# Kernel optimization log

Hardware: AMD Instinct MI355X
Metric: run time of the kernel (lower is better)

Reference implementation:

```python
import jax, jax.numpy as jnp
import numpy as np

N = 100000      # nodes
E = 800000      # edges (avg degree 8)
D_IN = 128
D_OUT = 128
HOPS = 3        # K in SGConv


def setup_inputs() -> dict:
    key = jax.random.key(0)
    k1, k2, k3 = jax.random.split(key, 3)
    x = jax.random.normal(k1, (N, D_IN), dtype=jnp.float32)
    edge_index = jax.random.randint(k2, (2, E), 0, N, dtype=jnp.int64)
    # SGConv's final torch.nn.Linear(in_channels, out_channels)
    W = jax.random.normal(k3, (D_OUT, D_IN), dtype=jnp.float32) / np.sqrt(D_IN).astype(np.float32)
    b = jnp.zeros((D_OUT,), dtype=jnp.float32)
    return {"x": x, "edge_index": edge_index, "W": W, "b": b}


def reference(x, edge_index, W, b):
    n = x.shape[0]
    loop = jnp.arange(n, dtype=edge_index.dtype)
    # gcn_norm with add_self_loops=True (SGConv default)
    src = jnp.concatenate([edge_index[0], loop])  # message sources
    dst = jnp.concatenate([edge_index[1], loop])  # aggregation targets
    ones = jnp.ones(src.shape[0], dtype=x.dtype)
    deg = jax.ops.segment_sum(ones, dst, num_segments=n)
    dinv = jnp.where(deg > 0, jax.lax.rsqrt(deg), 0.0)
    norm = dinv[src] * dinv[dst]  # symmetric D^-1/2 A_hat D^-1/2 coefficients

    def hop(h, _):
        msg = h[src] * norm[:, None]                      # [E+N, D] gather
        return jax.ops.segment_sum(msg, dst, num_segments=n), None

    h, _ = jax.lax.scan(hop, x, None, length=HOPS)        # A_norm^K x
    return h @ W.T + b                                     # final linear
```

## Files before the change

kernel.cpp:

```cpp
#include <hip/hip_runtime.h>
#include <hip/hip_bf16.h>

#define DF 128


typedef __attribute__((ext_vector_type(8))) short shortx8;
typedef __attribute__((ext_vector_type(4))) float floatx4;

__device__ __forceinline__ unsigned short f32_to_bf16_rne(float f) {
    unsigned int u = __float_as_uint(f);
    unsigned int r = (u >> 16) & 1u;
    u += 0x7FFFu + r;
    return (unsigned short)(u >> 16);
}
__device__ __forceinline__ float bf16_lo(unsigned int w) { return __uint_as_float(w << 16); }
__device__ __forceinline__ float bf16_hi(unsigned int w) { return __uint_as_float(w & 0xffff0000u); }
__device__ __forceinline__ unsigned int pack_bf16(float x, float y) {
    return ((unsigned int)f32_to_bf16_rne(y) << 16) | (unsigned int)f32_to_bf16_rne(x);
}

__global__ void detect_flags_kernel(const unsigned int* __restrict__ ew, int enwords,
                                    const unsigned short* __restrict__ xh, int xnh,
                                    int* __restrict__ flagI, int* __restrict__ flagD) {
    __shared__ int eodd_nz;
    __shared__ int xbig;
    if (threadIdx.x == 0) { eodd_nz = 0; xbig = 0; }
    __syncthreads();
    int f1 = 0;
    for (int i = 1 + 2 * (int)threadIdx.x; i < enwords; i += 2 * (int)blockDim.x)
        if (ew[i] != 0u) f1 = 1;
    int c = 0;
    for (int i = 2 * (int)threadIdx.x; i < xnh; i += 2 * (int)blockDim.x) {
        unsigned int e = ((unsigned int)xh[i] >> 7) & 0xFFu;
        if (e >= 0xC0u) c++;
    }
    if (f1) eodd_nz = 1;
    if (c) atomicAdd(&xbig, c);
    __syncthreads();
    if (threadIdx.x == 0) {
        *flagI = (eodd_nz == 0) ? 1 : 0;
        *flagD = (xbig > 8) ? 0 : 1;
    }
}

__global__ __launch_bounds__(256) void prep_kernel(
        const int* __restrict__ eidx, const int* __restrict__ flagI,
        const int* __restrict__ flagD, int E, int n,
        int* __restrict__ cnt, int* __restrict__ rank,
        const void* __restrict__ x, uint2* __restrict__ xb, int nw2,
        const void* __restrict__ W, const void* __restrict__ b,
        unsigned short* __restrict__ Wb, float* __restrict__ bias_f,
        int g1, int g2) {
    int bid = (int)blockIdx.x;
    if (bid < g1) {
        int t = bid * 256 + (int)threadIdx.x;
        int base = t * 4;
        if (base >= E) return;
        int isI64 = *flagI;
        const long long* p64 = (const long long*)eidx;
        int s[4], d[4];
#pragma unroll
        for (int j = 0; j < 4; ++j) {
            int e = base + j;
            if (e < E) {
                if (isI64) { s[j] = (int)p64[e]; d[j] = (int)p64[(long long)E + e]; }
                else       { s[j] = eidx[e];     d[j] = eidx[E + e]; }
            } else { s[j] = -1; d[j] = -1; }
        }
        int r[4];
#pragma unroll
        for (int j = 0; j < 4; ++j) {
            bool ok = ((unsigned)d[j] < (unsigned)n) && ((unsigned)s[j] < (unsigned)n);
            r[j] = ok ? atomicAdd(&cnt[d[j]], 1) : 0;
        }
        if (base + 3 < E) {
            *(int4*)&rank[base] = make_int4(r[0], r[1], r[2], r[3]);
        } else {
#pragma unroll
            for (int j = 0; j < 4; ++j)
                if (base + j < E) rank[base + j] = r[j];
        }
    } else if (bid < g1 + g2) {
        int i = (bid - g1) * 256 + (int)threadIdx.x;
        if (i >= nw2) return;
        if (*flagD) {
            xb[i] = ((const uint2*)x)[i];
        } else {
            float4 v = ((const float4*)x)[i];
            uint2 o;
            o.x = pack_bf16(v.x, v.y);
            o.y = pack_bf16(v.z, v.w);
            xb[i] = o;
        }
    } else {
        int i = (bid - g1 - g2) * 256 + (int)threadIdx.x;
        int bf = *flagD;
        if (i < 128 * 128)
            Wb[i] = bf ? ((const unsigned short*)W)[i] : f32_to_bf16_rne(((const float*)W)[i]);
        if (i < 128)
            bias_f[i] = bf ? bf16_lo((unsigned int)((const unsigned short*)b)[i]) : ((const float*)b)[i];
    }
}

__global__ void scan_blocks_kernel(const int* __restrict__ cnt, int* __restrict__ row_start,
                                   int* __restrict__ partials, int n) {
    __shared__ int s[256];
    int i = blockIdx.x * 256 + threadIdx.x;
    int v = (i < n) ? cnt[i] : 0;
    s[threadIdx.x] = v;
    __syncthreads();
    for (int off = 1; off < 256; off <<= 1) {
        int t = ((int)threadIdx.x >= off) ? s[threadIdx.x - off] : 0;
        __syncthreads();
        s[threadIdx.x] += t;
        __syncthreads();
    }
    if (i < n) row_start[i] = s[threadIdx.x] - v;
    if (threadIdx.x == 255) partials[blockIdx.x] = s[255];
}

__global__ void scan_partials_kernel(int* __restrict__ partials, int nparts) {
    __shared__ int s[512];
    int v = ((int)threadIdx.x < nparts) ? partials[threadIdx.x] : 0;
    s[threadIdx.x] = v;
    __syncthreads();
    for (int off = 1; off < 512; off <<= 1) {
        int t = ((int)threadIdx.x >= off) ? s[threadIdx.x - off] : 0;
        __syncthreads();
        s[threadIdx.x] += t;
        __syncthreads();
    }
    if ((int)threadIdx.x < nparts) partials[threadIdx.x] = s[threadIdx.x] - v;
}

__global__ void finalize_rows_kernel(int* __restrict__ row_start, const int* __restrict__ partials,
                                     const int* __restrict__ cnt, float* __restrict__ dinv, int n) {
    int i = blockIdx.x * 256 + threadIdx.x;
    if (i < n) {
        int r = row_start[i] + partials[blockIdx.x];
        row_start[i] = r;
        dinv[i] = rsqrtf((float)(cnt[i] + 1));
        if (i == n - 1) row_start[n] = r + cnt[i];
    }
}

__global__ __launch_bounds__(256) void scatter_kernel(const int* __restrict__ eidx,
                                                      const int* __restrict__ flagI,
                                                      const int* __restrict__ rank,
                                                      const int* __restrict__ row_start,
                                                      int E, int n, const float* __restrict__ dinv,
                                                      int2* __restrict__ csr) {
    int t = blockIdx.x * blockDim.x + threadIdx.x;
    int base = t * 4;
    if (base >= E) return;
    int isI64 = *flagI;
    const long long* p64 = (const long long*)eidx;
    int s[4], d[4], r[4];
    if (base + 3 < E) {
        int4 rv = *(const int4*)&rank[base];
        r[0] = rv.x; r[1] = rv.y; r[2] = rv.z; r[3] = rv.w;
#pragma unroll
        for (int j = 0; j < 4; ++j) {
            int e = base + j;
            if (isI64) { s[j] = (int)p64[e]; d[j] = (int)p64[(long long)E + e]; }
            else       { s[j] = eidx[e];     d[j] = eidx[E + e]; }
        }
    } else {
#pragma unroll
        for (int j = 0; j < 4; ++j) {
            int e = base + j;
            if (e < E) {
                r[j] = rank[e];
                if (isI64) { s[j] = (int)p64[e]; d[j] = (int)p64[(long long)E + e]; }
                else       { s[j] = eidx[e];     d[j] = eidx[E + e]; }
            } else { s[j] = -1; d[j] = -1; r[j] = 0; }
        }
    }
#pragma unroll
    for (int j = 0; j < 4; ++j) {
        bool ok = ((unsigned)d[j] < (unsigned)n) && ((unsigned)s[j] < (unsigned)n);
        if (ok) {
            int pos = row_start[d[j]] + r[j];
            int2 pk;
            pk.x = s[j];
            pk.y = __float_as_int(dinv[s[j]]);
            csr[pos] = pk;
        }
    }
}

__global__ __launch_bounds__(256) void hop_kernel(const uint4* __restrict__ hin,
                                                  uint4* __restrict__ hout,
                                                  const int2* __restrict__ csr,
                                                  const int* __restrict__ row_start,
                                                  const float* __restrict__ dinv, int n) {
    int gw = (int)((blockIdx.x * 256 + threadIdx.x) >> 6);
    int lane = (int)(threadIdx.x & 63);
    if (gw >= n) return;
    int e = lane >> 4, c = lane & 15;
    float di = dinv[gw];
    int beg = row_start[gw], end = row_start[gw + 1];
    uint4 sv = hin[(size_t)gw * 16 + c];
    float a0 = 0.f, a1 = 0.f, a2 = 0.f, a3 = 0.f, a4 = 0.f, a5 = 0.f, a6 = 0.f, a7 = 0.f;
    for (int j = beg + e; j < end; j += 8) {
        int2 ed0 = csr[j];
        bool has1 = (j + 4) < end;
        int2 ed1 = has1 ? csr[j + 4] : ed0;
        uint4 v0 = hin[(size_t)ed0.x * 16 + c];
        uint4 v1 = hin[(size_t)ed1.x * 16 + c];
        float w0 = __int_as_float(ed0.y);
        float w1 = has1 ? __int_as_float(ed1.y) : 0.f;
        a0 += w0 * bf16_lo(v0.x); a1 += w0 * bf16_hi(v0.x);
        a2 += w0 * bf16_lo(v0.y); a3 += w0 * bf16_hi(v0.y);
        a4 += w0 * bf16_lo(v0.z); a5 += w0 * bf16_hi(v0.z);
        a6 += w0 * bf16_lo(v0.w); a7 += w0 * bf16_hi(v0.w);
        a0 += w1 * bf16_lo(v1.x); a1 += w1 * bf16_hi(v1.x);
        a2 += w1 * bf16_lo(v1.y); a3 += w1 * bf16_hi(v1.y);
        a4 += w1 * bf16_lo(v1.z); a5 += w1 * bf16_hi(v1.z);
        a6 += w1 * bf16_lo(v1.w); a7 += w1 * bf16_hi(v1.w);
    }
    a0 += __shfl_xor(a0, 16); a0 += __shfl_xor(a0, 32);
    a1 += __shfl_xor(a1, 16); a1 += __shfl_xor(a1, 32);
    a2 += __shfl_xor(a2, 16); a2 += __shfl_xor(a2, 32);
    a3 += __shfl_xor(a3, 16); a3 += __shfl_xor(a3, 32);
    a4 += __shfl_xor(a4, 16); a4 += __shfl_xor(a4, 32);
    a5 += __shfl_xor(a5, 16); a5 += __shfl_xor(a5, 32);
    a6 += __shfl_xor(a6, 16); a6 += __shfl_xor(a6, 32);
    a7 += __shfl_xor(a7, 16); a7 += __shfl_xor(a7, 32);
    a0 = di * (a0 + di * bf16_lo(sv.x)); a1 = di * (a1 + di * bf16_hi(sv.x));
    a2 = di * (a2 + di * bf16_lo(sv.y)); a3 = di * (a3 + di * bf16_hi(sv.y));
    a4 = di * (a4 + di * bf16_lo(sv.z)); a5 = di * (a5 + di * bf16_hi(sv.z));
    a6 = di * (a6 + di * bf16_lo(sv.w)); a7 = di * (a7 + di * bf16_hi(sv.w));
    if (e == 0) {
        uint4 o;
        o.x = pack_bf16(a0, a1);
        o.y = pack_bf16(a2, a3);
        o.z = pack_bf16(a4, a5);
        o.w = pack_bf16(a6, a7);
        hout[(size_t)gw * 16 + c] = o;
    }
}

__global__ __launch_bounds__(256, 2) void linear_mfma_kernel(
        const unsigned short* __restrict__ h, const unsigned short* __restrict__ Wb,
        const float* __restrict__ bias_f, void* __restrict__ out,
        const int* __restrict__ flagD, int n) {
    int bf = *flagD;
    int wave = (int)(threadIdx.x >> 6);
    int lane = (int)(threadIdx.x & 63);
    int q = lane >> 4, m16 = lane & 15;

    shortx8 bfrag[8][4];
    float bias[8];
#pragma unroll
    for (int nt = 0; nt < 8; ++nt) {
        int wr = nt * 16 + m16;
#pragma unroll
        for (int t = 0; t < 4; ++t)
            bfrag[nt][t] = *(const shortx8*)&Wb[wr * 128 + t * 32 + q * 8];
        bias[nt] = bias_f[wr];
    }

    int nstrips = (n + 15) / 16;
    int wid = (int)blockIdx.x * 4 + wave;
    int nw = (int)gridDim.x * 4;
    for (int s = wid; s < nstrips; s += nw) {
        int row0 = s * 16;
        int arow = row0 + m16;
        if (arow >= n) arow = n - 1;
        shortx8 afrag[4];
#pragma unroll
        for (int t = 0; t < 4; ++t)
            afrag[t] = *(const shortx8*)&h[(size_t)arow * 128 + t * 32 + q * 8];

        floatx4 acc[8];
#pragma unroll
        for (int nt = 0; nt < 8; ++nt) acc[nt] = (floatx4){0.f, 0.f, 0.f, 0.f};
#pragma unroll
        for (int t = 0; t < 4; ++t)
#pragma unroll
            for (int nt = 0; nt < 8; ++nt)
                acc[nt] = __builtin_amdgcn_mfma_f32_16x16x32_bf16(afrag[t], bfrag[nt][t], acc[nt], 0, 0, 0);

#pragma unroll
        for (int nt = 0; nt < 8; ++nt)
#pragma unroll
            for (int r = 0; r < 4; ++r) {
                int row = row0 + q * 4 + r;
                if (row < n) {
                    float v = acc[nt][r] + bias[nt];
                    size_t oi = (size_t)row * 128 + nt * 16 + m16;
                    if (bf) ((unsigned short*)out)[oi] = f32_to_bf16_rne(v);
                    else    ((float*)out)[oi] = v;
                }
            }
    }
}

extern "C" void kernel_launch(void* const* d_in, const int* in_sizes, int n_in,
                              void* d_out, int out_size, void* d_ws, size_t ws_size,
                              hipStream_t stream) {
    const void* x = d_in[0];
    const int* eidx = (const int*)d_in[1];
    const void* W = d_in[2];
    const void* b = d_in[3];

    int n = in_sizes[0] / DF;
    int E = in_sizes[1] / 2;

    char* ws = (char*)d_ws;
    size_t off = 0;
    auto alloc = [&](size_t bytes) -> void* {
        void* p = ws + off;
        off = (off + bytes + 255) & ~(size_t)255;
        return p;
    };
    unsigned int* hb = (unsigned int*)alloc((size_t)n * 64 * 4);
    float* dinv      = (float*)alloc((size_t)n * 4);
    int*   cnt       = (int*)alloc((size_t)n * 4);
    int*   row_start = (int*)alloc((size_t)(n + 1) * 4);
    int*   partials  = (int*)alloc(4096);
    int*   flagI     = (int*)alloc(256);
    int*   flagD     = (int*)alloc(256);
    unsigned short* Wb = (unsigned short*)alloc(128 * 128 * 2);
    float* bias_f    = (float*)alloc(128 * 4);
    int2*  csr       = (int2*)alloc((size_t)E * 8);
    int*   rank      = (int*)alloc((size_t)E * 4);
    unsigned int* xb = (unsigned int*)d_out;

    hipMemsetAsync(cnt, 0, (size_t)n * 4, stream);

    int enw = 8192; if (2 * E < enw) enw = 2 * E;
    int xnh = 16384; if (n * DF < xnh) xnh = n * DF;
    detect_flags_kernel<<<1, 256, 0, stream>>>((const unsigned int*)eidx, enw,
                                               (const unsigned short*)x, xnh, flagI, flagD);

    int nb = (n + 255) / 256;
    int e4 = (E + 3) / 4;
    int g1 = (e4 + 255) / 256;
    int nw2 = n * 32;
    int g2 = (nw2 + 255) / 256;
    int g3 = 64;

    prep_kernel<<<g1 + g2 + g3, 256, 0, stream>>>(
        eidx, flagI, flagD, E, n, cnt, rank, x, (uint2*)xb, nw2,
        W, b, Wb, bias_f, g1, g2);

    scan_blocks_kernel<<<nb, 256, 0, stream>>>(cnt, row_start, partials, n);
    scan_partials_kernel<<<1, 512, 0, stream>>>(partials, nb);
    finalize_rows_kernel<<<nb, 256, 0, stream>>>(row_start, partials, cnt, dinv, n);
    scatter_kernel<<<g1, 256, 0, stream>>>(eidx, flagI, rank, row_start, E, n, dinv, csr);

    int hb_grid = (n + 3) / 4;
    hop_kernel<<<hb_grid, 256, 0, stream>>>((const uint4*)xb, (uint4*)hb, csr, row_start, dinv, n);
    hop_kernel<<<hb_grid, 256, 0, stream>>>((const uint4*)hb, (uint4*)xb, csr, row_start, dinv, n);
    hop_kernel<<<hb_grid, 256, 0, stream>>>((const uint4*)xb, (uint4*)hb, csr, row_start, dinv, n);

    int nstrips = (n + 15) / 16;
    int lgrid = 512; if ((nstrips + 3) / 4 < lgrid) lgrid = (nstrips + 3) / 4;
    linear_mfma_kernel<<<lgrid, 256, 0, stream>>>(
        (const unsigned short*)hb, Wb, bias_f, d_out, flagD, n);
}
```

Before: 317.2 us.

## Replace CSR build with fixed-capacity per-node buckets plus overflow fixup

Edges are written straight into a padded per-destination slot array of 32 entries, using the atomic rank taken while counting degrees. This removes the prefix-scan kernels, the row_start array and the separate scatter pass. The hop kernel now computes normalisation weights on the fly from the degree counts, which adds an extra gather of cnt[src] per edge. Edges beyond capacity go to an overflow list that a single-block fixup kernel applies serially after each hop; this adds three small launches and an extra bf16 rounding on overflowed rows.

New measurement: 319.1 us. No clear change (+0.6%).

```diff
diff --git a/kernel.cpp b/kernel.cpp
--- a/kernel.cpp
+++ b/kernel.cpp
@@ -2,6 +2,8 @@
 #include <hip/hip_bf16.h>
 
 #define DF 128
+#define CAP 32
+#define OVF_CAP 65536
 
 
 typedef __attribute__((ext_vector_type(8))) short shortx8;
@@ -46,7 +48,8 @@
 __global__ __launch_bounds__(256) void prep_kernel(
         const int* __restrict__ eidx, const int* __restrict__ flagI,
         const int* __restrict__ flagD, int E, int n,
-        int* __restrict__ cnt, int* __restrict__ rank,
+        int* __restrict__ cnt, int* __restrict__ csrF,
+        int2* __restrict__ ovf, int* __restrict__ ovf_cnt,
         const void* __restrict__ x, uint2* __restrict__ xb, int nw2,
         const void* __restrict__ W, const void* __restrict__ b,
         unsigned short* __restrict__ Wb, float* __restrict__ bias_f,
@@ -71,14 +74,17 @@
 #pragma unroll
         for (int j = 0; j < 4; ++j) {
             bool ok = ((unsigned)d[j] < (unsigned)n) && ((unsigned)s[j] < (unsigned)n);
-            r[j] = ok ? atomicAdd(&cnt[d[j]], 1) : 0;
-        }
-        if (base + 3 < E) {
-            *(int4*)&rank[base] = make_int4(r[0], r[1], r[2], r[3]);
-        } else {
-#pragma unroll
-            for (int j = 0; j < 4; ++j)
-                if (base + j < E) rank[base + j] = r[j];
+            r[j] = ok ? atomicAdd(&cnt[d[j]], 1) : -1;
+        }
+#pragma unroll
+        for (int j = 0; j < 4; ++j) {
+            if (r[j] < 0) continue;
+            if (r[j] < CAP) {
+                csrF[d[j] * CAP + r[j]] = s[j];
+            } else {
+                int p = atomicAdd(ovf_cnt, 1);
+                if (p < OVF_CAP) ovf[p] = make_int2(s[j], d[j]);
+            }
         }
     } else if (bid < g1 + g2) {
         int i = (bid - g1) * 256 + (int)threadIdx.x;
@@ -102,114 +108,29 @@
     }
 }
 
-__global__ void scan_blocks_kernel(const int* __restrict__ cnt, int* __restrict__ row_start,
-                                   int* __restrict__ partials, int n) {
-    __shared__ int s[256];
-    int i = blockIdx.x * 256 + threadIdx.x;
-    int v = (i < n) ? cnt[i] : 0;
-    s[threadIdx.x] = v;
-    __syncthreads();
-    for (int off = 1; off < 256; off <<= 1) {
-        int t = ((int)threadIdx.x >= off) ? s[threadIdx.x - off] : 0;
-        __syncthreads();
-        s[threadIdx.x] += t;
-        __syncthreads();
-    }
-    if (i < n) row_start[i] = s[threadIdx.x] - v;
-    if (threadIdx.x == 255) partials[blockIdx.x] = s[255];
-}
-
-__global__ void scan_partials_kernel(int* __restrict__ partials, int nparts) {
-    __shared__ int s[512];
-    int v = ((int)threadIdx.x < nparts) ? partials[threadIdx.x] : 0;
-    s[threadIdx.x] = v;
-    __syncthreads();
-    for (int off = 1; off < 512; off <<= 1) {
-        int t = ((int)threadIdx.x >= off) ? s[threadIdx.x - off] : 0;
-        __syncthreads();
-        s[threadIdx.x] += t;
-        __syncthreads();
-    }
-    if ((int)threadIdx.x < nparts) partials[threadIdx.x] = s[threadIdx.x] - v;
-}
-
-__global__ void finalize_rows_kernel(int* __restrict__ row_start, const int* __restrict__ partials,
-                                     const int* __restrict__ cnt, float* __restrict__ dinv, int n) {
-    int i = blockIdx.x * 256 + threadIdx.x;
-    if (i < n) {
-        int r = row_start[i] + partials[blockIdx.x];
-        row_start[i] = r;
-        dinv[i] = rsqrtf((float)(cnt[i] + 1));
-        if (i == n - 1) row_start[n] = r + cnt[i];
-    }
-}
-
-__global__ __launch_bounds__(256) void scatter_kernel(const int* __restrict__ eidx,
-                                                      const int* __restrict__ flagI,
-                                                      const int* __restrict__ rank,
-                                                      const int* __restrict__ row_start,
-                                                      int E, int n, const float* __restrict__ dinv,
-                                                      int2* __restrict__ csr) {
-    int t = blockIdx.x * blockDim.x + threadIdx.x;
-    int base = t * 4;
-    if (base >= E) return;
-    int isI64 = *flagI;
-    const long long* p64 = (const long long*)eidx;
-    int s[4], d[4], r[4];
-    if (base + 3 < E) {
-        int4 rv = *(const int4*)&rank[base];
-        r[0] = rv.x; r[1] = rv.y; r[2] = rv.z; r[3] = rv.w;
-#pragma unroll
-        for (int j = 0; j < 4; ++j) {
-            int e = base + j;
-            if (isI64) { s[j] = (int)p64[e]; d[j] = (int)p64[(long long)E + e]; }
-            else       { s[j] = eidx[e];     d[j] = eidx[E + e]; }
-        }
-    } else {
-#pragma unroll
-        for (int j = 0; j < 4; ++j) {
-            int e = base + j;
-            if (e < E) {
-                r[j] = rank[e];
-                if (isI64) { s[j] = (int)p64[e]; d[j] = (int)p64[(long long)E + e]; }
-                else       { s[j] = eidx[e];     d[j] = eidx[E + e]; }
-            } else { s[j] = -1; d[j] = -1; r[j] = 0; }
-        }
-    }
-#pragma unroll
-    for (int j = 0; j < 4; ++j) {
-        bool ok = ((unsigned)d[j] < (unsigned)n) && ((unsigned)s[j] < (unsigned)n);
-        if (ok) {
-            int pos = row_start[d[j]] + r[j];
-            int2 pk;
-            pk.x = s[j];
-            pk.y = __float_as_int(dinv[s[j]]);
-            csr[pos] = pk;
-        }
-    }
-}
-
 __global__ __launch_bounds__(256) void hop_kernel(const uint4* __restrict__ hin,
                                                   uint4* __restrict__ hout,
-                                                  const int2* __restrict__ csr,
-                                                  const int* __restrict__ row_start,
-                                                  const float* __restrict__ dinv, int n) {
+                                                  const int* __restrict__ csrF,
+                                                  const int* __restrict__ cnt, int n) {
     int gw = (int)((blockIdx.x * 256 + threadIdx.x) >> 6);
     int lane = (int)(threadIdx.x & 63);
     if (gw >= n) return;
     int e = lane >> 4, c = lane & 15;
-    float di = dinv[gw];
-    int beg = row_start[gw], end = row_start[gw + 1];
+    int cv = cnt[gw];
+    float di = rsqrtf((float)(cv + 1));
+    int beg = gw * CAP;
+    int len = cv < CAP ? cv : CAP;
+    int end = beg + len;
     uint4 sv = hin[(size_t)gw * 16 + c];
     float a0 = 0.f, a1 = 0.f, a2 = 0.f, a3 = 0.f, a4 = 0.f, a5 = 0.f, a6 = 0.f, a7 = 0.f;
     for (int j = beg + e; j < end; j += 8) {
-        int2 ed0 = csr[j];
+        int s0 = csrF[j];
         bool has1 = (j + 4) < end;
-        int2 ed1 = has1 ? csr[j + 4] : ed0;
-        uint4 v0 = hin[(size_t)ed0.x * 16 + c];
-        uint4 v1 = hin[(size_t)ed1.x * 16 + c];
-        float w0 = __int_as_float(ed0.y);
-        float w1 = has1 ? __int_as_float(ed1.y) : 0.f;
+        int s1 = has1 ? csrF[j + 4] : s0;
+        uint4 v0 = hin[(size_t)s0 * 16 + c];
+        uint4 v1 = hin[(size_t)s1 * 16 + c];
+        float w0 = rsqrtf((float)(cnt[s0] + 1));
+        float w1 = has1 ? rsqrtf((float)(cnt[s1] + 1)) : 0.f;
         a0 += w0 * bf16_lo(v0.x); a1 += w0 * bf16_hi(v0.x);
         a2 += w0 * bf16_lo(v0.y); a3 += w0 * bf16_hi(v0.y);
         a4 += w0 * bf16_lo(v0.z); a5 += w0 * bf16_hi(v0.z);
@@ -241,6 +162,25 @@
     }
 }
 
+__global__ void fixup_kernel(const unsigned int* __restrict__ hin,
+                             unsigned int* __restrict__ hout,
+                             const int2* __restrict__ ovf, const int* __restrict__ ovf_cnt,
+                             const int* __restrict__ cnt) {
+    int m = *ovf_cnt;
+    if (m > OVF_CAP) m = OVF_CAP;
+    int t = (int)threadIdx.x;
+    for (int i = 0; i < m; ++i) {
+        int2 sd = ovf[i];
+        float w  = rsqrtf((float)(cnt[sd.x] + 1));
+        float dd = rsqrtf((float)(cnt[sd.y] + 1));
+        unsigned int hv = hin[(size_t)sd.x * 64 + t];
+        unsigned int ov = hout[(size_t)sd.y * 64 + t];
+        float lo = bf16_lo(ov) + dd * w * bf16_lo(hv);
+        float hi = bf16_hi(ov) + dd * w * bf16_hi(hv);
+        hout[(size_t)sd.y * 64 + t] = pack_bf16(lo, hi);
+    }
+}
+
 __global__ __launch_bounds__(256, 2) void linear_mfma_kernel(
         const unsigned short* __restrict__ h, const unsigned short* __restrict__ Wb,
         const float* __restrict__ bias_f, void* __restrict__ out,
@@ -316,26 +256,24 @@
         return p;
     };
     unsigned int* hb = (unsigned int*)alloc((size_t)n * 64 * 4);
-    float* dinv      = (float*)alloc((size_t)n * 4);
     int*   cnt       = (int*)alloc((size_t)n * 4);
-    int*   row_start = (int*)alloc((size_t)(n + 1) * 4);
-    int*   partials  = (int*)alloc(4096);
     int*   flagI     = (int*)alloc(256);
     int*   flagD     = (int*)alloc(256);
     unsigned short* Wb = (unsigned short*)alloc(128 * 128 * 2);
     float* bias_f    = (float*)alloc(128 * 4);
-    int2*  csr       = (int2*)alloc((size_t)E * 8);
-    int*   rank      = (int*)alloc((size_t)E * 4);
+    int*   csrF      = (int*)alloc((size_t)n * CAP * 4);
+    int2*  ovf       = (int2*)alloc((size_t)OVF_CAP * 8);
+    int*   ovf_cnt   = (int*)alloc(256);
     unsigned int* xb = (unsigned int*)d_out;
 
     hipMemsetAsync(cnt, 0, (size_t)n * 4, stream);
+    hipMemsetAsync(ovf_cnt, 0, 4, stream);
 
     int enw = 8192; if (2 * E < enw) enw = 2 * E;
     int xnh = 16384; if (n * DF < xnh) xnh = n * DF;
     detect_flags_kernel<<<1, 256, 0, stream>>>((const unsigned int*)eidx, enw,
                                                (const unsigned short*)x, xnh, flagI, flagD);
 
-    int nb = (n + 255) / 256;
     int e4 = (E + 3) / 4;
     int g1 = (e4 + 255) / 256;
     int nw2 = n * 32;
@@ -343,18 +281,16 @@
     int g3 = 64;
 
     prep_kernel<<<g1 + g2 + g3, 256, 0, stream>>>(
-        eidx, flagI, flagD, E, n, cnt, rank, x, (uint2*)xb, nw2,
-        W, b, Wb, bias_f, g1, g2);
-
-    scan_blocks_kernel<<<nb, 256, 0, stream>>>(cnt, row_start, partials, n);
-    scan_partials_kernel<<<1, 512, 0, stream>>>(partials, nb);
-    finalize_rows_kernel<<<nb, 256, 0, stream>>>(row_start, partials, cnt, dinv, n);
-    scatter_kernel<<<g1, 256, 0, stream>>>(eidx, flagI, rank, row_start, E, n, dinv, csr);
+        eidx, flagI, flagD, E, n, cnt, csrF, ovf, ovf_cnt,
+        x, (uint2*)xb, nw2, W, b, Wb, bias_f, g1, g2);
 
     int hb_grid = (n + 3) / 4;
-    hop_kernel<<<hb_grid, 256, 0, stream>>>((const uint4*)xb, (uint4*)hb, csr, row_start, dinv, n);
-    hop_kernel<<<hb_grid, 256, 0, stream>>>((const uint4*)hb, (uint4*)xb, csr, row_start, dinv, n);
-    hop_kernel<<<hb_grid, 256, 0, stream>>>((const uint4*)xb, (uint4*)hb, csr, row_start, dinv, n);
+    hop_kernel<<<hb_grid, 256, 0, stream>>>((const uint4*)xb, (uint4*)hb, csrF, cnt, n);
+    fixup_kernel<<<1, 64, 0, stream>>>((const unsigned int*)xb, hb, ovf, ovf_cnt, cnt);
+    hop_kernel<<<hb_grid, 256, 0, stream>>>((const uint4*)hb, (uint4*)xb, csrF, cnt, n);
+    fixup_kernel<<<1, 64, 0, stream>>>((const unsigned int*)hb, xb, ovf, ovf_cnt, cnt);
+    hop_kernel<<<hb_grid, 256, 0, stream>>>((const uint4*)xb, (uint4*)hb, csrF, cnt, n);
+    fixup_kernel<<<1, 64, 0, stream>>>((const unsigned int*)xb, hb, ovf, ovf_cnt, cnt);
 
     int nstrips = (n + 15) / 16;
     int lgrid = 512; if ((nstrips + 3) / 4 < lgrid) lgrid = (nstrips + 3) / 4;
```
